# Performance work log

Hardware: AMD Instinct MI355X
Metric: run time of the kernel (lower is better)

## Reference

```python
import jax, jax.numpy as jnp
import numpy as np

EPS = 1e-5
GROUPS = 32


def setup_inputs() -> dict:
    key = jax.random.key(0)
    ks = jax.random.split(key, 12)
    b, c, h, w = 8, 256, 64, 64
    s = 1.0 / np.sqrt(c)
    return {
        "x": jax.random.normal(ks[0], (b, c, h, w), jnp.float32),
        "gn_w": jax.random.uniform(ks[1], (c,), jnp.float32, 0.5, 1.5),
        "gn_b": jax.random.normal(ks[2], (c,), jnp.float32) * 0.1,
        "wq": jax.random.normal(ks[3], (c, c), jnp.float32) * s,
        "bq": jax.random.normal(ks[4], (c,), jnp.float32) * 0.02,
        "wk": jax.random.normal(ks[5], (c, c), jnp.float32) * s,
        "bk": jax.random.normal(ks[6], (c,), jnp.float32) * 0.02,
        "wv": jax.random.normal(ks[7], (c, c), jnp.float32) * s,
        "bv": jax.random.normal(ks[8], (c,), jnp.float32) * 0.02,
        "wp": jax.random.normal(ks[9], (c, c), jnp.float32) * s,
        "bp": jax.random.normal(ks[10], (c,), jnp.float32) * 0.02,
        "gamma": jax.random.normal(ks[11], (1,), jnp.float32),
    }


def _group_norm(x, weight, bias):
    b, c, h, w = x.shape
    g = min(c, GROUPS)
    xg = x.reshape(b, g, c // g, h * w)
    mean = xg.mean(axis=(2, 3), keepdims=True)
    var = jnp.var(xg, axis=(2, 3), keepdims=True)
    xn = (xg - mean) * jax.lax.rsqrt(var + EPS)
    xn = xn.reshape(b, c, h, w)
    return xn * weight[None, :, None, None] + bias[None, :, None, None]


def reference(x, gn_w, gn_b, wq, bq, wk, bk, wv, bv, wp, bp, gamma):
    b, c, h, w = x.shape
    x_dash = _group_norm(x, gn_w, gn_b)           # (b,c,h,w)
    xf = x_dash.reshape(b, c, h * w)              # (b,c,n)
    # 1x1 convs == per-pixel linear maps over channels
    q = jnp.einsum('oc,bcn->bon', wq, xf) + bq[None, :, None]
    k = jnp.einsum('oc,bcn->bon', wk, xf) + bk[None, :, None]
    v = jnp.einsum('oc,bcn->bon', wv, xf) + bv[None, :, None]
    # attn[b,i,j] = <q[:,i], k[:,j]> / sqrt(c)
    attn = jnp.einsum('bci,bcj->bij', q, k) / jnp.sqrt(jnp.asarray(c, x.dtype))
    attn = jax.nn.softmax(attn, axis=-1)
    # out[b,c,i] = sum_j v[b,c,j] * attn[b,i,j]
    out = jnp.einsum('bcj,bij->bci', v, attn)
    out = jnp.einsum('oc,bcn->bon', wp, out) + bp[None, :, None]
    out = out.reshape(b, c, h, w)
    return x + gamma[0] * out
```

## Files before the change

kernel.cpp:

```cpp
#include <hip/hip_runtime.h>
#include <cstdint>
#include <cstddef>


#define NB   8
#define NC   256
#define NPIX 4096
#define CPG  8

typedef __attribute__((ext_vector_type(8))) short bf16x8;
typedef __attribute__((ext_vector_type(4))) short s16x4;
typedef __attribute__((ext_vector_type(8))) short s16x8;
typedef __attribute__((ext_vector_type(4))) float f32x4;

__device__ __forceinline__ short f2bf(float f) {
  union { float f; uint32_t u; } v; v.f = f;
  return (short)((v.u + 0x7fffu + ((v.u >> 16) & 1u)) >> 16);
}

__device__ __forceinline__ uint32_t cvtpk_bf(float a, float b) {
  uint32_t r;
  asm("v_cvt_pk_bf16_f32 %0, %1, %2" : "=v"(r) : "v"(a), "v"(b));
  return r;
}

__device__ __forceinline__ f32x4 mfma16(bf16x8 a, bf16x8 b, f32x4 c) {
  return __builtin_amdgcn_mfma_f32_16x16x32_bf16(a, b, c, 0, 0, 0);
}

__device__ __forceinline__ void gload_lds16(const short* g, short* l) {
  __builtin_amdgcn_global_load_lds(
      (const __attribute__((address_space(1))) void*)g,
      (__attribute__((address_space(3))) void*)l, 16, 0, 0);
}

__global__ __launch_bounds__(256) void wconv4(
    const float* __restrict__ w0, const float* __restrict__ w1,
    const float* __restrict__ w2, const float* __restrict__ w3,
    short* __restrict__ o0, short* __restrict__ o1,
    short* __restrict__ o2, short* __restrict__ o3) {
  int m = blockIdx.x >> 6;
  const float* w = (m == 0) ? w0 : (m == 1) ? w1 : (m == 2) ? w2 : w3;
  short* o = (m == 0) ? o0 : (m == 1) ? o1 : (m == 2) ? o2 : o3;
  int i = ((blockIdx.x & 63) * 256 + threadIdx.x) * 4;
  float4 v = *reinterpret_cast<const float4*>(w + i);
  s16x4 p;
  p[0] = f2bf(v.x); p[1] = f2bf(v.y); p[2] = f2bf(v.z); p[3] = f2bf(v.w);
  *reinterpret_cast<s16x4*>(o + i) = p;
}

__global__ __launch_bounds__(256) void gnorm(const float* __restrict__ x,
                                             const float* __restrict__ gw,
                                             const float* __restrict__ gb,
                                             short* __restrict__ xdt) {
  int b = blockIdx.x >> 5;
  int g = blockIdx.x & 31;
  const float* xp = x + ((size_t)b * NC + (size_t)g * CPG) * NPIX;
  int t = threadIdx.x;

  float s = 0.f, ss = 0.f;
  const float4* xp4 = reinterpret_cast<const float4*>(xp);
  for (int i = t; i < (CPG * NPIX) / 4; i += 256) {
    float4 v = xp4[i];
    s  += v.x + v.y + v.z + v.w;
    ss += v.x * v.x + v.y * v.y + v.z * v.z + v.w * v.w;
  }
  for (int m = 32; m; m >>= 1) { s += __shfl_xor(s, m); ss += __shfl_xor(ss, m); }
  __shared__ float red[10];
  int wid = t >> 6;
  if ((t & 63) == 0) { red[wid] = s; red[4 + wid] = ss; }
  __syncthreads();
  if (t == 0) {
    float a  = red[0] + red[1] + red[2] + red[3];
    float b2 = red[4] + red[5] + red[6] + red[7];
    float mean = a * (1.f / 32768.f);
    float var  = b2 * (1.f / 32768.f) - mean * mean;
    red[8] = mean;
    red[9] = rsqrtf(var + 1e-5f);
  }
  __syncthreads();
  float mean = red[8], rstd = red[9];

  float wv2[CPG], bv2[CPG];
  for (int cc = 0; cc < CPG; ++cc) {
    float wgt = gw[g * CPG + cc] * rstd;
    wv2[cc] = wgt;
    bv2[cc] = gb[g * CPG + cc] - mean * wgt;
  }
  for (int pix = t; pix < NPIX; pix += 256) {
    s16x8 pk;
    for (int cc = 0; cc < CPG; ++cc)
      pk[cc] = f2bf(fmaf(xp[cc * NPIX + pix], wv2[cc], bv2[cc]));
    *reinterpret_cast<s16x8*>(&xdt[((size_t)b * NPIX + pix) * NC + g * CPG]) = pk;
  }
}

__global__ __launch_bounds__(256) void qkv_gemm(
    const short* __restrict__ wq_bf, const short* __restrict__ wk_bf,
    const short* __restrict__ wv_bf,
    const float* __restrict__ bq, const float* __restrict__ bk,
    const float* __restrict__ bv,
    const short* __restrict__ xdt,
    short* __restrict__ qt, short* __restrict__ kt, short* __restrict__ vv) {
  int nt = blockIdx.x, b = blockIdx.y, mi = blockIdx.z;
  const short* W; const float* bia;
  if (mi == 0)      { W = wq_bf; bia = bq; }
  else if (mi == 1) { W = wk_bf; bia = bk; }
  else              { W = wv_bf; bia = bv; }

  __shared__ short xtile[64 * 256];
  __shared__ float bias_lds[256];
  int t = threadIdx.x;
  const short* xg = xdt + ((size_t)b * NPIX + nt * 64) * NC;
  for (int it = 0; it < 8; ++it) {
    int id = t + it * 256, row = id >> 5, part = id & 31;
    *reinterpret_cast<uint4*>(&xtile[row * 256 + (part ^ (row & 7)) * 8]) =
        *reinterpret_cast<const uint4*>(&xg[(size_t)row * 256 + part * 8]);
  }
  bias_lds[t] = bia[t];
  __syncthreads();

  int w = t >> 6, lane = t & 63, g = lane >> 4, lr = lane & 15;
  f32x4 acc[4][4];
  f32x4 zz = {0.f, 0.f, 0.f, 0.f};
  for (int i = 0; i < 4; ++i) for (int j = 0; j < 4; ++j) acc[i][j] = zz;

  for (int c0 = 0; c0 < 256; c0 += 32) {
    bf16x8 af[4], bfr[4];
    for (int mf = 0; mf < 4; ++mf)
      af[mf] = *reinterpret_cast<const bf16x8*>(
          &W[(size_t)(w * 64 + mf * 16 + lr) * 256 + c0 + g * 8]);
    for (int nf = 0; nf < 4; ++nf) {
      int row = nf * 16 + lr;
      bfr[nf] = *reinterpret_cast<const bf16x8*>(
          &xtile[row * 256 + (((c0 >> 3) + g) ^ (row & 7)) * 8]);
    }
    for (int mf = 0; mf < 4; ++mf)
      for (int nf = 0; nf < 4; ++nf)
        acc[mf][nf] = mfma16(af[mf], bfr[nf], acc[mf][nf]);
  }

  if (mi < 2) {
    short* outp = (mi == 0) ? qt : kt;
    for (int mf = 0; mf < 4; ++mf)
      for (int nf = 0; nf < 4; ++nf) {
        int ob = w * 64 + mf * 16 + g * 4;
        int n  = nt * 64 + nf * 16 + lr;
        s16x4 pk;
        for (int r = 0; r < 4; ++r)
          pk[r] = f2bf(acc[mf][nf][r] + bias_lds[ob + r]);
        *reinterpret_cast<s16x4*>(&outp[((size_t)b * NPIX + n) * NC + ob]) = pk;
      }
  } else {
    for (int mf = 0; mf < 4; ++mf)
      for (int nf = 0; nf < 4; ++nf) {
        int ob = w * 64 + mf * 16 + g * 4;
        int n  = nt * 64 + nf * 16 + lr;
        for (int r = 0; r < 4; ++r)
          vv[((size_t)b * NC + ob + r) * NPIX + n] =
              f2bf(acc[mf][nf][r] + bias_lds[ob + r]);
      }
  }
}

__global__ __launch_bounds__(256, 2) void attn(
    const short* __restrict__ qt, const short* __restrict__ kt,
    const short* __restrict__ vv, short* __restrict__ ot) {
  int b = blockIdx.x, itile = blockIdx.y;
  __shared__ short ktile[2][64 * 256];
  __shared__ short Pb[64 * 72];
  __shared__ float alpha_lds[64];
  __shared__ float lsum_lds[64];

  int t = threadIdx.x, w = t >> 6, lane = t & 63, g = lane >> 4, lr = lane & 15;
  int i0 = itile * 64;

  const short* ktg = kt + (size_t)b * NPIX * NC;
  const short* vg  = vv + (size_t)b * NC * NPIX;

  for (int it = 0; it < 8; ++it) {
    int id = it * 256 + t, row = id >> 5, ch = id & 31;
    gload_lds16(&ktg[(size_t)row * 256 + (ch ^ (row & 7)) * 8],
                &ktile[0][id * 8]);
  }

  bf16x8 qf[8];
  {
    const short* qrow = qt + ((size_t)b * NPIX + i0 + w * 16 + lr) * NC;
    for (int ks = 0; ks < 8; ++ks)
      qf[ks] = *reinterpret_cast<const bf16x8*>(&qrow[ks * 32 + g * 8]);
  }

  f32x4 zz = {0.f, 0.f, 0.f, 0.f};
  f32x4 oacc[4][4];
  for (int i = 0; i < 4; ++i) for (int j = 0; j < 4; ++j) oacc[i][j] = zz;
  float m_ = -1e30f, l_ = 0.f;

  const float sc = 0.0625f, L2E = 1.44269504f;
  const float SCL = sc * L2E;

  for (int jt = 0; jt < 64; ++jt) {
    int cur = jt & 1;

    bf16x8 va[2][4];
    for (int ks2 = 0; ks2 < 2; ++ks2)
      for (int mf = 0; mf < 4; ++mf)
        va[ks2][mf] = *reinterpret_cast<const bf16x8*>(
            &vg[(size_t)(w * 64 + mf * 16 + lr) * NPIX + jt * 64 + ks2 * 32 + g * 8]);

    asm volatile("s_waitcnt vmcnt(8)" ::: "memory");
    __builtin_amdgcn_s_barrier();
    asm volatile("" ::: "memory");

    {
      const short* kg2 = ktg + (size_t)((jt + 1) & 63) * 64 * 256;
      short* lb = &ktile[cur ^ 1][0];
      for (int it = 0; it < 8; ++it) {
        int id = it * 256 + t, row = id >> 5, ch = id & 31;
        gload_lds16(&kg2[row * 256 + (ch ^ (row & 7)) * 8], &lb[id * 8]);
      }
    }

    f32x4 s[4];
    for (int mf = 0; mf < 4; ++mf) s[mf] = zz;
    const short* kts = &ktile[cur][0];
    __builtin_amdgcn_s_setprio(1);
    for (int ks = 0; ks < 8; ++ks) {
      bf16x8 kf[4];
      for (int mf = 0; mf < 4; ++mf) {
        int row = mf * 16 + lr;
        kf[mf] = *reinterpret_cast<const bf16x8*>(
            &kts[row * 256 + (((ks * 4) + g) ^ (row & 7)) * 8]);
      }
      for (int mf = 0; mf < 4; ++mf) s[mf] = mfma16(kf[mf], qf[ks], s[mf]);
    }
    __builtin_amdgcn_s_setprio(0);

    float mx = s[0][0];
    for (int mf = 0; mf < 4; ++mf)
      for (int r = 0; r < 4; ++r) mx = fmaxf(mx, s[mf][r]);
    mx = fmaxf(mx, __shfl_xor(mx, 16));
    mx = fmaxf(mx, __shfl_xor(mx, 32));
    float pm = mx * sc;
    float mn = (pm - m_ <= 8.f) ? m_ : pm;
    float alpha = exp2f((m_ - mn) * L2E);
    float mnl = mn * L2E;
    float ps = 0.f;
    int q_loc = w * 16 + lr;
    for (int mf = 0; mf < 4; ++mf) {
      float p0 = exp2f(fmaf(s[mf][0], SCL, -mnl));
      float p1 = exp2f(fmaf(s[mf][1], SCL, -mnl));
      float p2 = exp2f(fmaf(s[mf][2], SCL, -mnl));
      float p3 = exp2f(fmaf(s[mf][3], SCL, -mnl));
      ps += p0 + p1 + p2 + p3;
      uint2 pk;
      pk.x = cvtpk_bf(p0, p1);
      pk.y = cvtpk_bf(p2, p3);
      *reinterpret_cast<uint2*>(&Pb[q_loc * 72 + mf * 16 + g * 4]) = pk;
    }
    ps += __shfl_xor(ps, 16);
    ps += __shfl_xor(ps, 32);
    l_ = l_ * alpha + ps;
    m_ = mn;
    if (lane < 16) alpha_lds[w * 16 + lane] = alpha;

    asm volatile("s_waitcnt lgkmcnt(0)" ::: "memory");
    __builtin_amdgcn_s_barrier();
    asm volatile("" ::: "memory");

    asm volatile("s_waitcnt vmcnt(8)" ::: "memory");

    float av[4];
    for (int nf = 0; nf < 4; ++nf) av[nf] = alpha_lds[nf * 16 + lr];
    if (__any((av[0] != 1.f) | (av[1] != 1.f) | (av[2] != 1.f) | (av[3] != 1.f))) {
      for (int mf = 0; mf < 4; ++mf)
        for (int nf = 0; nf < 4; ++nf) oacc[mf][nf] *= av[nf];
    }

    __builtin_amdgcn_s_setprio(1);
    for (int ks2 = 0; ks2 < 2; ++ks2) {
      bf16x8 pb[4];
      for (int nf = 0; nf < 4; ++nf)
        pb[nf] = *reinterpret_cast<const bf16x8*>(
            &Pb[(nf * 16 + lr) * 72 + ks2 * 32 + g * 8]);
      for (int mf = 0; mf < 4; ++mf)
        for (int nf = 0; nf < 4; ++nf)
          oacc[mf][nf] = mfma16(va[ks2][mf], pb[nf], oacc[mf][nf]);
    }
    __builtin_amdgcn_s_setprio(0);
  }

  if (lane < 16) lsum_lds[w * 16 + lane] = l_;
  __syncthreads();

  for (int nf = 0; nf < 4; ++nf) {
    float inv = 1.f / lsum_lds[nf * 16 + lr];
    int i = i0 + nf * 16 + lr;
    for (int mf = 0; mf < 4; ++mf) {
      int cb = w * 64 + mf * 16 + g * 4;
      s16x4 pk;
      for (int r = 0; r < 4; ++r) pk[r] = f2bf(oacc[mf][nf][r] * inv);
      *reinterpret_cast<s16x4*>(&ot[((size_t)b * NPIX + i) * NC + cb]) = pk;
    }
  }
}

__global__ __launch_bounds__(256) void proj_res(
    const short* __restrict__ wp_bf, const float* __restrict__ bp,
    const short* __restrict__ ot, const float* __restrict__ x,
    const float* __restrict__ gamma, float* __restrict__ out) {
  int nt = blockIdx.x, b = blockIdx.y;
  __shared__ short otile[64 * 256];
  __shared__ float bias_lds[256];
  int t = threadIdx.x;
  const short* og = ot + ((size_t)b * NPIX + nt * 64) * NC;
  for (int itx = 0; itx < 8; ++itx) {
    int id = t + itx * 256, row = id >> 5, part = id & 31;
    *reinterpret_cast<uint4*>(&otile[row * 256 + (part ^ (row & 7)) * 8]) =
        *reinterpret_cast<const uint4*>(&og[(size_t)row * 256 + part * 8]);
  }
  bias_lds[t] = bp[t];
  __syncthreads();

  int w = t >> 6, lane = t & 63, g = lane >> 4, lr = lane & 15;
  f32x4 acc[4][4];
  f32x4 zz = {0.f, 0.f, 0.f, 0.f};
  for (int i = 0; i < 4; ++i) for (int j = 0; j < 4; ++j) acc[i][j] = zz;

  for (int c0 = 0; c0 < 256; c0 += 32) {
    bf16x8 af[4], bfr[4];
    for (int mf = 0; mf < 4; ++mf)
      af[mf] = *reinterpret_cast<const bf16x8*>(
          &wp_bf[(size_t)(w * 64 + mf * 16 + lr) * 256 + c0 + g * 8]);
    for (int nf = 0; nf < 4; ++nf) {
      int row = nf * 16 + lr;
      bfr[nf] = *reinterpret_cast<const bf16x8*>(
          &otile[row * 256 + (((c0 >> 3) + g) ^ (row & 7)) * 8]);
    }
    for (int mf = 0; mf < 4; ++mf)
      for (int nf = 0; nf < 4; ++nf)
        acc[mf][nf] = mfma16(af[mf], bfr[nf], acc[mf][nf]);
  }

  float gm = gamma[0];
  for (int mf = 0; mf < 4; ++mf)
    for (int nf = 0; nf < 4; ++nf) {
      int ob = w * 64 + mf * 16 + g * 4;
      int n  = nt * 64 + nf * 16 + lr;
      for (int r = 0; r < 4; ++r) {
        size_t idx = ((size_t)b * NC + ob + r) * NPIX + n;
        out[idx] = x[idx] + gm * (acc[mf][nf][r] + bias_lds[ob + r]);
      }
    }
}

extern "C" void kernel_launch(void* const* d_in, const int* in_sizes, int n_in,
                              void* d_out, int out_size, void* d_ws, size_t ws_size,
                              hipStream_t stream) {
  (void)in_sizes; (void)n_in; (void)out_size; (void)ws_size;
  const float* x     = (const float*)d_in[0];
  const float* gn_w  = (const float*)d_in[1];
  const float* gn_b  = (const float*)d_in[2];
  const float* wq    = (const float*)d_in[3];
  const float* bq    = (const float*)d_in[4];
  const float* wk    = (const float*)d_in[5];
  const float* bk    = (const float*)d_in[6];
  const float* wv    = (const float*)d_in[7];
  const float* bv    = (const float*)d_in[8];
  const float* wp    = (const float*)d_in[9];
  const float* bp    = (const float*)d_in[10];
  const float* gamma = (const float*)d_in[11];
  float* out = (float*)d_out;

  char* ws = (char*)d_ws;
  const size_t WSZ = 131072;
  const size_t TSZ = (size_t)NB * NPIX * NC * 2;
  short* wq_bf = (short*)(ws);
  short* wk_bf = (short*)(ws + WSZ);
  short* wv_bf = (short*)(ws + 2 * WSZ);
  short* wp_bf = (short*)(ws + 3 * WSZ);
  short* xdt   = (short*)(ws + 4 * WSZ);
  short* qt    = (short*)(ws + 4 * WSZ + TSZ);
  short* kt    = (short*)(ws + 4 * WSZ + 2 * TSZ);
  short* vv    = (short*)(ws + 4 * WSZ + 3 * TSZ);
  short* ot    = xdt;

  wconv4<<<256, 256, 0, stream>>>(wq, wk, wv, wp, wq_bf, wk_bf, wv_bf, wp_bf);

  gnorm<<<256, 256, 0, stream>>>(x, gn_w, gn_b, xdt);

  qkv_gemm<<<dim3(64, 8, 3), 256, 0, stream>>>(wq_bf, wk_bf, wv_bf, bq, bk, bv,
                                               xdt, qt, kt, vv);

  attn<<<dim3(8, 64), 256, 0, stream>>>(qt, kt, vv, ot);

  proj_res<<<dim3(64, 8), 256, 0, stream>>>(wp_bf, bp, ot, x, gamma, out);
}
```

Measured before the change: 309.3 us.

## Software-pipeline PV matmul behind next QK and single-buffer K tile

Restructures the attention loop so the P·V MFMAs for the previous key tile run at the top of the next iteration, overlapping with that iteration's QK work. P and alpha move into double-buffered LDS with an XOR-swizzled P layout, while K drops to a single LDS buffer that is reloaded after a mid-iteration barrier. This cuts LDS use and the number of barriers on the critical path. In exchange, the K prefetch only overlaps with the softmax, since each iteration now waits for all loads to finish. On the last iteration the prefetch reads one tile past the batch's K data, which for the final batch runs past the end of the buffer.

```diff
diff --git a/kernel.cpp b/kernel.cpp
--- a/kernel.cpp
+++ b/kernel.cpp
@@ -167,22 +167,20 @@
     const short* __restrict__ qt, const short* __restrict__ kt,
     const short* __restrict__ vv, short* __restrict__ ot) {
   int b = blockIdx.x, itile = blockIdx.y;
-  __shared__ short ktile[2][64 * 256];
-  __shared__ short Pb[64 * 72];
-  __shared__ float alpha_lds[64];
-  __shared__ float lsum_lds[64];
+  __shared__ short ktile[64 * 256];
+  __shared__ short Pb[2][64 * 64];
+  __shared__ float alpha_lds[2][64];
 
   int t = threadIdx.x, w = t >> 6, lane = t & 63, g = lane >> 4, lr = lane & 15;
   int i0 = itile * 64;
 
   const short* ktg = kt + (size_t)b * NPIX * NC;
-  const short* vg  = vv + (size_t)b * NC * NPIX;
 
   for (int it = 0; it < 8; ++it) {
     int id = it * 256 + t, row = id >> 5, ch = id & 31;
-    gload_lds16(&ktg[(size_t)row * 256 + (ch ^ (row & 7)) * 8],
-                &ktile[0][id * 8]);
-  }
+    gload_lds16(ktg + row * 256 + (ch ^ (row & 7)) * 8, &ktile[id * 8]);
+  }
+  const short* kgp = ktg + 16384;
 
   bf16x8 qf[8];
   {
@@ -191,50 +189,83 @@
       qf[ks] = *reinterpret_cast<const bf16x8*>(&qrow[ks * 32 + g * 8]);
   }
 
+  const short* vp = vv + (size_t)b * NC * NPIX + (size_t)(w * 64 + lr) * NPIX + g * 8;
+
+  int q_loc = w * 16 + lr;
+  int pw[4];
+  for (int mf = 0; mf < 4; ++mf)
+    pw[mf] = q_loc * 64 + (((mf * 2 + (g >> 1)) ^ (q_loc & 7)) * 8) + (g & 1) * 4;
+  int pr[4][2];
+  for (int nf = 0; nf < 4; ++nf)
+    for (int ks2 = 0; ks2 < 2; ++ks2) {
+      int qq = nf * 16 + lr;
+      pr[nf][ks2] = qq * 64 + (((ks2 * 4 + g) ^ (qq & 7)) * 8);
+    }
+
   f32x4 zz = {0.f, 0.f, 0.f, 0.f};
   f32x4 oacc[4][4];
   for (int i = 0; i < 4; ++i) for (int j = 0; j < 4; ++j) oacc[i][j] = zz;
+  bf16x8 va[2][4];
   float m_ = -1e30f, l_ = 0.f;
 
   const float sc = 0.0625f, L2E = 1.44269504f;
   const float SCL = sc * L2E;
 
   for (int jt = 0; jt < 64; ++jt) {
-    int cur = jt & 1;
-
-    bf16x8 va[2][4];
+    int cur = jt & 1, prv = cur ^ 1;
+
+    asm volatile("s_waitcnt vmcnt(0) lgkmcnt(0)" ::: "memory");
+    __builtin_amdgcn_s_barrier();
+    asm volatile("" ::: "memory");
+
+    if (jt > 0) {
+      float av[4];
+      for (int nf = 0; nf < 4; ++nf) av[nf] = alpha_lds[prv][nf * 16 + lr];
+      if (__any((av[0] != 1.f) | (av[1] != 1.f) | (av[2] != 1.f) | (av[3] != 1.f))) {
+        for (int mf = 0; mf < 4; ++mf)
+          for (int nf = 0; nf < 4; ++nf) oacc[mf][nf] *= av[nf];
+      }
+      __builtin_amdgcn_s_setprio(1);
+      for (int ks2 = 0; ks2 < 2; ++ks2) {
+        bf16x8 pb[4];
+        for (int nf = 0; nf < 4; ++nf)
+          pb[nf] = *reinterpret_cast<const bf16x8*>(&Pb[prv][pr[nf][ks2]]);
+        for (int mf = 0; mf < 4; ++mf)
+          for (int nf = 0; nf < 4; ++nf)
+            oacc[mf][nf] = mfma16(va[ks2][mf], pb[nf], oacc[mf][nf]);
+      }
+      __builtin_amdgcn_s_setprio(0);
+    }
+
     for (int ks2 = 0; ks2 < 2; ++ks2)
       for (int mf = 0; mf < 4; ++mf)
         va[ks2][mf] = *reinterpret_cast<const bf16x8*>(
-            &vg[(size_t)(w * 64 + mf * 16 + lr) * NPIX + jt * 64 + ks2 * 32 + g * 8]);
-
-    asm volatile("s_waitcnt vmcnt(8)" ::: "memory");
-    __builtin_amdgcn_s_barrier();
-    asm volatile("" ::: "memory");
-
-    {
-      const short* kg2 = ktg + (size_t)((jt + 1) & 63) * 64 * 256;
-      short* lb = &ktile[cur ^ 1][0];
-      for (int it = 0; it < 8; ++it) {
-        int id = it * 256 + t, row = id >> 5, ch = id & 31;
-        gload_lds16(&kg2[row * 256 + (ch ^ (row & 7)) * 8], &lb[id * 8]);
-      }
-    }
+            vp + (size_t)mf * (16 * NPIX) + ks2 * 32);
+    vp += 64;
 
     f32x4 s[4];
     for (int mf = 0; mf < 4; ++mf) s[mf] = zz;
-    const short* kts = &ktile[cur][0];
     __builtin_amdgcn_s_setprio(1);
     for (int ks = 0; ks < 8; ++ks) {
       bf16x8 kf[4];
       for (int mf = 0; mf < 4; ++mf) {
         int row = mf * 16 + lr;
         kf[mf] = *reinterpret_cast<const bf16x8*>(
-            &kts[row * 256 + (((ks * 4) + g) ^ (row & 7)) * 8]);
+            &ktile[row * 256 + (((ks * 4) + g) ^ (row & 7)) * 8]);
       }
       for (int mf = 0; mf < 4; ++mf) s[mf] = mfma16(kf[mf], qf[ks], s[mf]);
     }
     __builtin_amdgcn_s_setprio(0);
+
+    asm volatile("s_waitcnt lgkmcnt(0)" ::: "memory");
+    __builtin_amdgcn_s_barrier();
+    asm volatile("" ::: "memory");
+
+    for (int it = 0; it < 8; ++it) {
+      int id = it * 256 + t, row = id >> 5, ch = id & 31;
+      gload_lds16(kgp + row * 256 + (ch ^ (row & 7)) * 8, &ktile[id * 8]);
+    }
+    kgp += 16384;
 
     float mx = s[0][0];
     for (int mf = 0; mf < 4; ++mf)
@@ -246,7 +277,6 @@
     float alpha = exp2f((m_ - mn) * L2E);
     float mnl = mn * L2E;
     float ps = 0.f;
-    int q_loc = w * 16 + lr;
     for (int mf = 0; mf < 4; ++mf) {
       float p0 = exp2f(fmaf(s[mf][0], SCL, -mnl));
       float p1 = exp2f(fmaf(s[mf][1], SCL, -mnl));
@@ -256,45 +286,40 @@
       uint2 pk;
       pk.x = cvtpk_bf(p0, p1);
       pk.y = cvtpk_bf(p2, p3);
-      *reinterpret_cast<uint2*>(&Pb[q_loc * 72 + mf * 16 + g * 4]) = pk;
+      *reinterpret_cast<uint2*>(&Pb[cur][pw[mf]]) = pk;
     }
     ps += __shfl_xor(ps, 16);
     ps += __shfl_xor(ps, 32);
     l_ = l_ * alpha + ps;
     m_ = mn;
-    if (lane < 16) alpha_lds[w * 16 + lane] = alpha;
-
-    asm volatile("s_waitcnt lgkmcnt(0)" ::: "memory");
-    __builtin_amdgcn_s_barrier();
-    asm volatile("" ::: "memory");
-
-    asm volatile("s_waitcnt vmcnt(8)" ::: "memory");
-
+    if (lane < 16) alpha_lds[cur][w * 16 + lane] = alpha;
+  }
+
+  asm volatile("s_waitcnt vmcnt(0) lgkmcnt(0)" ::: "memory");
+  __builtin_amdgcn_s_barrier();
+  asm volatile("" ::: "memory");
+  {
     float av[4];
-    for (int nf = 0; nf < 4; ++nf) av[nf] = alpha_lds[nf * 16 + lr];
+    for (int nf = 0; nf < 4; ++nf) av[nf] = alpha_lds[1][nf * 16 + lr];
     if (__any((av[0] != 1.f) | (av[1] != 1.f) | (av[2] != 1.f) | (av[3] != 1.f))) {
       for (int mf = 0; mf < 4; ++mf)
         for (int nf = 0; nf < 4; ++nf) oacc[mf][nf] *= av[nf];
     }
-
-    __builtin_amdgcn_s_setprio(1);
     for (int ks2 = 0; ks2 < 2; ++ks2) {
       bf16x8 pb[4];
       for (int nf = 0; nf < 4; ++nf)
-        pb[nf] = *reinterpret_cast<const bf16x8*>(
-            &Pb[(nf * 16 + lr) * 72 + ks2 * 32 + g * 8]);
+        pb[nf] = *reinterpret_cast<const bf16x8*>(&Pb[1][pr[nf][ks2]]);
       for (int mf = 0; mf < 4; ++mf)
         for (int nf = 0; nf < 4; ++nf)
           oacc[mf][nf] = mfma16(va[ks2][mf], pb[nf], oacc[mf][nf]);
     }
-    __builtin_amdgcn_s_setprio(0);
-  }
-
-  if (lane < 16) lsum_lds[w * 16 + lane] = l_;
+  }
+
+  if (lane < 16) alpha_lds[0][w * 16 + lane] = l_;
   __syncthreads();
 
   for (int nf = 0; nf < 4; ++nf) {
-    float inv = 1.f / lsum_lds[nf * 16 + lr];
+    float inv = 1.f / alpha_lds[0][nf * 16 + lr];
     int i = i0 + nf * 16 + lr;
     for (int mf = 0; mf < 4; ++mf) {
       int cb = w * 64 + mf * 16 + g * 4;
```

New measurement: 307.1 us. No clear change (-0.7%).
